# Performance work log

Hardware: AMD Instinct MI355X
Metric: run time of the kernel (lower is better)

Reference implementation:

```python
import jax, jax.numpy as jnp
import numpy as np

PATCH = 3
PAD = PATCH // 2  # stride = 1


def _extract_patches(x):
    """torch F.unfold(k=3, s=1, p=1) reshaped to [b, n=h*w, c*3*3] (c slowest, then ki, kj)."""
    b, c, h, w = x.shape
    xp = jnp.pad(x, ((0, 0), (0, 0), (PAD, PAD), (PAD, PAD)))
    # stack the 9 shifted views -> [b, c, 9, h, w]
    pats = jnp.stack([xp[:, :, i:i + h, j:j + w]
                      for i in range(PATCH) for j in range(PATCH)], axis=2)
    pats = pats.reshape(b, c, PATCH, PATCH, h, w)
    # -> [b, h*w, c*PATCH*PATCH], matching torch unfold channel ordering
    return pats.transpose(0, 4, 5, 1, 2, 3).reshape(b, h * w, c * PATCH * PATCH)


def _l2_normalize(x):
    # F.normalize(dim=2): x / max(||x||_2, 1e-12)
    n = jnp.linalg.norm(x, axis=2, keepdims=True)
    return x / jnp.maximum(n, 1e-12)


def _fold(patches_flat, c, h, w):
    """torch F.fold(k=3, s=1, p=1): overlap-add patches back to [b, c, h, w]."""
    b = patches_flat.shape[0]
    p = patches_flat.reshape(b, h, w, c, PATCH, PATCH)
    out = jnp.zeros((b, c, h + 2 * PAD, w + 2 * PAD), patches_flat.dtype)
    for i in range(PATCH):
        for j in range(PATCH):
            out = out.at[:, :, i:i + h, j:j + w].add(
                p[:, :, :, :, i, j].transpose(0, 3, 1, 2))
    return out[:, :, PAD:PAD + h, PAD:PAD + w]


def setup_inputs() -> dict:
    key = jax.random.key(0)
    k1, k2 = jax.random.split(key)
    B, C, H, W = 1, 256, 96, 96
    return {
        "content_features": jax.random.normal(k1, (B, C, H, W), dtype=jnp.float32),
        "style_features": jax.random.normal(k2, (B, C, H, W), dtype=jnp.float32),
    }


def reference(content_features, style_features):
    b, c, h, w = content_features.shape
    cpat = _extract_patches(content_features)   # [b, n, d]
    spat = _extract_patches(style_features)     # [b, m, d]
    # all-pairs cosine similarity: [b, n, m]
    sim = jnp.einsum('bnd,bmd->bnm', _l2_normalize(cpat), _l2_normalize(spat))
    best = jnp.argmax(sim, axis=2)              # [b, n]
    matched = jnp.take_along_axis(spat, best[:, :, None], axis=1)  # [b, n, d]
    num = _fold(matched, c, h, w)
    den = _fold(jnp.ones_like(matched), c, h, w)
    return num / (den + 1e-8)
```

## Files before the change

kernel.cpp:

```cpp
#include <hip/hip_runtime.h>

#define HH 96
#define WW 96
#define CCH 256
#define NPIX (HH*WW)
#define HP 98
#define NROWS 9604
#define CORE_LO 99
#define CORE_HI 9505

typedef unsigned short u16;
typedef short bf16x8 __attribute__((ext_vector_type(8)));
typedef float f32x4 __attribute__((ext_vector_type(4)));
typedef int i32x4 __attribute__((ext_vector_type(4)));

__device__ __forceinline__ f32x4 ld4u(const float* p) {
    f32x4 r; __builtin_memcpy(&r, p, 16); return r;
}
__device__ __forceinline__ i32x4 ld4ui(const int* p) {
    i32x4 r; __builtin_memcpy(&r, p, 16); return r;
}

__device__ __forceinline__ u16 f2bf_rne(float x) {
    unsigned u = __float_as_uint(x);
    return (u16)((u + 0x7FFFu + ((u >> 16) & 1u)) >> 16);
}

__device__ __forceinline__ void stage8(const u16* const* srcs, u16* dst, int kb) {
#pragma unroll
    for (int t = 0; t < 8; ++t)
        __builtin_amdgcn_global_load_lds(
            (const __attribute__((address_space(1))) unsigned int*)(srcs[t] + kb),
            (__attribute__((address_space(3))) unsigned int*)(dst + t * 512),
            16, 0, 0);
}

__global__ __launch_bounds__(256) void tobf16_kernel(const float* __restrict__ X,
                                                     u16* __restrict__ HiT,
                                                     u16* __restrict__ LoT) {
    __shared__ u16 hi[64][65], lo[64][65];
    const int n0 = blockIdx.x * 64, k0 = blockIdx.y * 64;
    const int t = threadIdx.x;
    {
        const int kr = t >> 6, nl = t & 63;
#pragma unroll
        for (int r = 0; r < 16; ++r) {
            int kl = kr * 16 + r;
            float x = X[(k0 + kl) * NPIX + n0 + nl];
            u16 h = f2bf_rne(x);
            float hf = __uint_as_float((unsigned)h << 16);
            hi[kl][nl] = h;
            lo[kl][nl] = f2bf_rne(x - hf);
        }
    }
    __syncthreads();
    {
        const int nr = t >> 6, kl = t & 63;
#pragma unroll
        for (int r = 0; r < 16; ++r) {
            int nl = nr * 16 + r;
            HiT[(n0 + nl) * CCH + k0 + kl] = hi[kl][nl];
            LoT[(n0 + nl) * CCH + k0 + kl] = lo[kl][nl];
        }
    }
}

__global__ __launch_bounds__(256) void xst_kernel(const float* __restrict__ X,
                                                  float* __restrict__ XT) {
    __shared__ float tile[64][65];
    const int p0 = blockIdx.x * 64, c0 = blockIdx.y * 64;
    const int t = threadIdx.x;
    const int rr = t >> 6, cl = t & 63;
#pragma unroll
    for (int r = 0; r < 16; ++r)
        tile[rr * 16 + r][cl] = X[(c0 + rr * 16 + r) * NPIX + p0 + cl];
    __syncthreads();
#pragma unroll
    for (int r = 0; r < 16; ++r)
        XT[(p0 + rr * 16 + r) * CCH + c0 + cl] = tile[cl][rr * 16 + r];
}

__global__ __launch_bounds__(256) void prep_kernel(const float* __restrict__ Xs,
                                                   float* __restrict__ ssum,
                                                   unsigned long long* __restrict__ keys) {
    int p = blockIdx.x * 256 + threadIdx.x;
    if (p >= NPIX) return;
    float s = 0.f;
#pragma unroll 8
    for (int c = 0; c < CCH; ++c) {
        float v = Xs[c * NPIX + p];
        s = fmaf(v, v, s);
    }
    ssum[p] = s;
    keys[p] = 0ULL;
}

__global__ __launch_bounds__(256) void rnsbp_kernel(const float* __restrict__ ssum,
                                                    float* __restrict__ rnsp,
                                                    float* __restrict__ biasp,
                                                    int* __restrict__ midxp) {
    int mp = blockIdx.x * 256 + threadIdx.x;
    if (mp >= 9632) return;
    int yq = mp / HP, xq = mp - yq * HP;
    bool real = (yq >= 1 && yq <= 96 && xq >= 1 && xq <= 96);
    if (!real) { rnsp[mp] = 0.f; biasp[mp] = -3e38f; midxp[mp] = 0; return; }
    int y = yq - 1, x = xq - 1;
    float s = 0.f;
    for (int dy = -1; dy <= 1; ++dy) {
        int yy = y + dy;
        if ((unsigned)yy >= HH) continue;
        for (int dx = -1; dx <= 1; ++dx) {
            int xx = x + dx;
            if ((unsigned)xx >= WW) continue;
            s += ssum[yy * WW + xx];
        }
    }
    rnsp[mp] = 1.f / fmaxf(sqrtf(s), 1e-12f);
    biasp[mp] = 0.f;
    midxp[mp] = y * WW + x;
}

__global__ __launch_bounds__(256) void padzero_kernel(float* __restrict__ cc, int wstride) {
    int p = blockIdx.x;
    int yq = p / HP, xq = p - yq * HP;
    if (yq >= 1 && yq <= 96 && xq >= 1 && xq <= 96) return;
    const f32x4 z = {0.f, 0.f, 0.f, 0.f};
    float* row = cc + (long long)p * wstride;
    for (int c = threadIdx.x * 4; c < wstride; c += 1024)
        *(f32x4*)&row[c] = z;
}

__global__ __launch_bounds__(256, 2) void cc_gemm_kernel(
        const u16* __restrict__ ChiT, const u16* __restrict__ CloT,
        const u16* __restrict__ ShiT, const u16* __restrict__ SloT,
        const u16* __restrict__ zbuf,
        float* __restrict__ cc, int csp, int wstride) {
    __shared__ u16 lds[2][4][8][64][8];

    const int tid = threadIdx.x;
    const int n0 = blockIdx.x * 128;
    const int m0 = blockIdx.y * 128;
    const int wave = tid >> 6, lane = tid & 63;
    const int wr = wave >> 1, wc = wave & 1;
    const int rlo = lane & 15, kseg = (lane >> 4) * 8;

    const u16* srcs[8];
    if (wave < 2) {
        const u16* base = (wave == 0) ? ChiT : CloT;
#pragma unroll
        for (int t = 0; t < 8; ++t)
            srcs[t] = base + (n0 + t * 16 + rlo) * CCH + kseg;
    } else {
        const u16* base = (wave == 2) ? ShiT : SloT;
#pragma unroll
        for (int t = 0; t < 8; ++t) {
            int qp = csp + m0 + t * 16 + rlo;
            int yq = qp / HP, xq = qp - yq * HP;
            bool ok = (qp < NROWS) && (yq >= 1 && yq <= 96 && xq >= 1 && xq <= 96);
            srcs[t] = ok ? (base + ((yq - 1) * WW + (xq - 1)) * CCH + kseg)
                         : (zbuf + kseg);
        }
    }
    u16* slab0 = &lds[0][wave][0][0][0];
    u16* slab1 = &lds[1][wave][0][0][0];

    f32x4 acc[4][4];
#pragma unroll
    for (int i = 0; i < 4; ++i)
#pragma unroll
        for (int j = 0; j < 4; ++j) acc[i][j] = (f32x4){0.f, 0.f, 0.f, 0.f};

    stage8(srcs, slab0, 0);
    stage8(srcs, slab1, 32);

#define READS(CUR)                                                          \
    bf16x8 ah[4], al[4], bh[4], bl[4];                                      \
    _Pragma("unroll")                                                       \
    for (int i = 0; i < 4; ++i) {                                           \
        ah[i] = *(const bf16x8*)&lds[CUR][0][wr * 4 + i][lane][0];          \
        al[i] = *(const bf16x8*)&lds[CUR][1][wr * 4 + i][lane][0];          \
        bh[i] = *(const bf16x8*)&lds[CUR][2][wc * 4 + i][lane][0];          \
        bl[i] = *(const bf16x8*)&lds[CUR][3][wc * 4 + i][lane][0];          \
    }

#define MFMAS                                                               \
    _Pragma("unroll")                                                       \
    for (int i = 0; i < 4; ++i)                                             \
        _Pragma("unroll")                                                   \
        for (int j = 0; j < 4; ++j) {                                       \
            acc[i][j] = __builtin_amdgcn_mfma_f32_16x16x32_bf16(ah[i], bh[j], acc[i][j], 0, 0, 0); \
            acc[i][j] = __builtin_amdgcn_mfma_f32_16x16x32_bf16(ah[i], bl[j], acc[i][j], 0, 0, 0); \
            acc[i][j] = __builtin_amdgcn_mfma_f32_16x16x32_bf16(al[i], bh[j], acc[i][j], 0, 0, 0); \
        }

#define KSTEP(KK, WN)                                                       \
    {                                                                       \
        asm volatile("s_waitcnt vmcnt(" #WN ")" ::: "memory");              \
        __builtin_amdgcn_sched_barrier(0);                                  \
        __builtin_amdgcn_s_barrier();                                       \
        READS((KK) & 1)                                                     \
        asm volatile("s_waitcnt lgkmcnt(0)" ::: "memory");                  \
        __builtin_amdgcn_sched_barrier(0);                                  \
        __builtin_amdgcn_s_barrier();                                       \
        if ((KK) + 2 < 8)                                                   \
            stage8(srcs, (((KK) & 1)) ? slab1 : slab0, ((KK) + 2) * 32);    \
        __builtin_amdgcn_sched_barrier(0);                                  \
        MFMAS                                                               \
    }

    KSTEP(0, 8) KSTEP(1, 8) KSTEP(2, 8) KSTEP(3, 8)
    KSTEP(4, 8) KSTEP(5, 8) KSTEP(6, 8) KSTEP(7, 0)

#undef KSTEP
#undef MFMAS
#undef READS

    const int r0 = (lane >> 4) * 4;
    const int cl = lane & 15;
#pragma unroll
    for (int i = 0; i < 4; ++i) {
        const int prow = n0 + wr * 64 + i * 16 + r0;
#pragma unroll
        for (int r = 0; r < 4; ++r) {
            const int row = prow + r;
            const int pp = row + 2 * (row / WW) + CORE_LO;
            const long long base = (long long)pp * wstride + m0 + wc * 64 + cl;
#pragma unroll
            for (int j = 0; j < 4; ++j)
                cc[base + j * 16] = acc[i][j][r];
        }
    }
}

__global__ __launch_bounds__(256) void boxsum_kernel(
        const float* __restrict__ cc, const float* __restrict__ rnsp,
        const float* __restrict__ biasp, const int* __restrict__ midxp,
        unsigned long long* __restrict__ keys,
        int core0, int coreEnd, int csp, int wstride) {
    const int wave = threadIdx.x >> 6, lane = threadIdx.x & 63;
    const int n = blockIdx.x * 4 + wave;
    const int pp = n + 2 * (n / WW) + CORE_LO;
    const long long rowbase = (long long)pp * wstride - csp;
    const int W1 = wstride + 1;

    const int OFF[9] = {-99, -98, -97, -1, 0, 1, 97, 98, 99};
    const float* tp[9];
#pragma unroll
    for (int t = 0; t < 9; ++t)
        tp[t] = cc + rowbase + core0 + lane * 4 + (long long)OFF[t] * W1;

    float best = -1e30f;
    int bidx = 0;
    for (int mq = core0 + lane * 4; mq < coreEnd; mq += 256) {
        f32x4 s = {0.f, 0.f, 0.f, 0.f};
#pragma unroll
        for (int t = 0; t < 9; ++t) { s += ld4u(tp[t]); tp[t] += 256; }
        f32x4 rv = ld4u(rnsp + mq);
        f32x4 bv = ld4u(biasp + mq);
        i32x4 iv = ld4ui(midxp + mq);
#pragma unroll
        for (int sl = 0; sl < 4; ++sl) {
            float v = fmaf(s[sl], rv[sl], bv[sl]);
            if (mq + sl >= coreEnd) v = -3e38f;
            if (v > best) { best = v; bidx = iv[sl]; }
        }
    }
#pragma unroll
    for (int d = 32; d; d >>= 1) {
        float ov = __shfl_xor(best, d);
        int oi = __shfl_xor(bidx, d);
        if (ov > best || (ov == best && oi < bidx)) { best = ov; bidx = oi; }
    }
    if (lane == 0) {
        unsigned u = __float_as_uint(best);
        unsigned key = (u & 0x80000000u) ? ~u : (u | 0x80000000u);
        unsigned long long k64 = ((unsigned long long)key << 32)
                               | (unsigned long long)(0xFFFFFFFFu - (unsigned)bidx);
        atomicMax(&keys[n], k64);
    }
}

__global__ __launch_bounds__(256) void fold2_kernel(const float* __restrict__ XsT,
                                                    const unsigned long long* __restrict__ keys,
                                                    float* __restrict__ outT) {
    const int wave = threadIdx.x >> 6, lane = threadIdx.x & 63;
    const int p = blockIdx.x * 4 + wave;
    const int y = p / WW, x = p - y * WW;
    f32x4 num = {0.f, 0.f, 0.f, 0.f};
    int den = 0;
#pragma unroll
    for (int i = 0; i < 3; ++i) {
        int ny = y + 1 - i;
        if ((unsigned)ny >= HH) continue;
#pragma unroll
        for (int j = 0; j < 3; ++j) {
            int nx = x + 1 - j;
            if ((unsigned)nx >= WW) continue;
            den++;
            unsigned long long k64 = keys[ny * WW + nx];
            int mg = (int)(0xFFFFFFFFu - (unsigned)(k64 & 0xFFFFFFFFu));
            int my = mg / WW, mx = mg - my * WW;
            int sy = my + i - 1, sx = mx + j - 1;
            if ((unsigned)sy < HH && (unsigned)sx < WW)
                num += ld4u(XsT + (long long)(sy * WW + sx) * CCH + lane * 4);
        }
    }
    float inv = 1.f / ((float)den + 1e-8f);
    f32x4 o = {num[0] * inv, num[1] * inv, num[2] * inv, num[3] * inv};
    *(f32x4*)&outT[(long long)p * CCH + lane * 4] = o;
}

__global__ __launch_bounds__(256) void outtr_kernel(const float* __restrict__ outT,
                                                    float* __restrict__ out) {
    __shared__ float tile[64][65];
    const int p0 = blockIdx.x * 64, c0 = blockIdx.y * 64;
    const int t = threadIdx.x;
    const int rr = t >> 6, cl = t & 63;
#pragma unroll
    for (int r = 0; r < 16; ++r)
        tile[rr * 16 + r][cl] = outT[(long long)(p0 + rr * 16 + r) * CCH + c0 + cl];
    __syncthreads();
#pragma unroll
    for (int r = 0; r < 16; ++r)
        out[(long long)(c0 + rr * 16 + r) * NPIX + p0 + cl] = tile[cl][rr * 16 + r];
}

extern "C" void kernel_launch(void* const* d_in, const int* in_sizes, int n_in,
                              void* d_out, int out_size, void* d_ws, size_t ws_size,
                              hipStream_t stream) {
    (void)in_sizes; (void)n_in; (void)out_size;
    const float* Xc = (const float*)d_in[0];
    const float* Xs = (const float*)d_in[1];
    float* out = (float*)d_out;

    char* w = (char*)d_ws;
    unsigned long long* keys = (unsigned long long*)w;  w += (size_t)NPIX * 8;
    float* ssum  = (float*)w;                           w += (size_t)NPIX * 4;
    float* rnsp  = (float*)w;                           w += (size_t)9632 * 4;
    float* biasp = (float*)w;                           w += (size_t)9632 * 4;
    int*   midxp = (int*)w;                             w += (size_t)9632 * 4;
    u16*   zbuf  = (u16*)w;                             w += 1024;
    float* XsT   = (float*)w;                           w += (size_t)NPIX * CCH * 4;
    float* outT  = (float*)w;                           w += (size_t)NPIX * CCH * 4;
    u16* ChiT = (u16*)w;                                w += (size_t)NPIX * CCH * 2;
    u16* CloT = (u16*)w;                                w += (size_t)NPIX * CCH * 2;
    u16* ShiT = (u16*)w;                                w += (size_t)NPIX * CCH * 2;
    u16* SloT = (u16*)w;                                w += (size_t)NPIX * CCH * 2;
    float* ccbuf = (float*)w;
    const size_t fixed = (size_t)(w - (char*)d_ws);

    long long avail = (ws_size > fixed + 4096)
                        ? (long long)(ws_size - fixed - 4096) : 0;
    int wstride = (int)(((avail / ((long long)NROWS * 4)) / 128) * 128);
    if (wstride > 2560) wstride = 2560;
    if (wstride < 512) wstride = 512;
    const int McCore = wstride - 198;

    hipMemsetAsync(zbuf, 0, 1024, stream);
    dim3 gt(NPIX / 64, CCH / 64);
    tobf16_kernel<<<gt, 256, 0, stream>>>(Xc, ChiT, CloT);
    tobf16_kernel<<<gt, 256, 0, stream>>>(Xs, ShiT, SloT);
    xst_kernel<<<gt, 256, 0, stream>>>(Xs, XsT);
    prep_kernel<<<NPIX / 256, 256, 0, stream>>>(Xs, ssum, keys);
    rnsbp_kernel<<<38, 256, 0, stream>>>(ssum, rnsp, biasp, midxp);
    padzero_kernel<<<NROWS, 256, 0, stream>>>(ccbuf, wstride);

    for (int core0 = CORE_LO; core0 < CORE_HI; core0 += McCore) {
        int coreEnd = (core0 + McCore < CORE_HI) ? core0 + McCore : CORE_HI;
        int csp = core0 - 99;
        int ce = coreEnd + 99; if (ce > NROWS) ce = NROWS;
        int Wc = ce - csp;
        dim3 g(NPIX / 128, (Wc + 127) / 128);
        cc_gemm_kernel<<<g, 256, 0, stream>>>(ChiT, CloT, ShiT, SloT, zbuf,
                                              ccbuf, csp, wstride);
        boxsum_kernel<<<NPIX / 4, 256, 0, stream>>>(ccbuf, rnsp, biasp, midxp, keys,
                                                    core0, coreEnd, csp, wstride);
    }

    fold2_kernel<<<NPIX / 4, 256, 0, stream>>>(XsT, keys, outT);
    outtr_kernel<<<gt, 256, 0, stream>>>(outT, out);
}
```

Measured before the change: 447.7 us.

## Use single-pass fp16 GEMM with candidate collection and exact fp32 rescoring

Replaces the three-MFMA bf16 hi/lo split GEMM with a single fp16 MFMA pass, which cuts GEMM compute and staging traffic by about two thirds and raises the occupancy hint. To keep the argmax exact, boxsum now records every style index whose approximate score lies within a content-norm-based threshold of the running max. A new rescore kernel then re-evaluates those candidates in fp32 and picks the best. The risks are candidate-list overflow beyond the cap of 64, fp16 range issues, and atomic contention in the candidate append path.

```diff
diff --git a/kernel.cpp b/kernel.cpp
--- a/kernel.cpp
+++ b/kernel.cpp
@@ -8,9 +8,11 @@
 #define NROWS 9604
 #define CORE_LO 99
 #define CORE_HI 9505
+#define CAND_CAP 64
 
 typedef unsigned short u16;
-typedef short bf16x8 __attribute__((ext_vector_type(8)));
+typedef _Float16 f16;
+typedef _Float16 f16x8 __attribute__((ext_vector_type(8)));
 typedef float f32x4 __attribute__((ext_vector_type(4)));
 typedef int i32x4 __attribute__((ext_vector_type(4)));
 
@@ -21,78 +23,50 @@
     i32x4 r; __builtin_memcpy(&r, p, 16); return r;
 }
 
-__device__ __forceinline__ u16 f2bf_rne(float x) {
-    unsigned u = __float_as_uint(x);
-    return (u16)((u + 0x7FFFu + ((u >> 16) & 1u)) >> 16);
-}
-
-__device__ __forceinline__ void stage8(const u16* const* srcs, u16* dst, int kb) {
-#pragma unroll
-    for (int t = 0; t < 8; ++t)
+__device__ __forceinline__ void stage4(const u16* const* srcs, u16* dst, int kb) {
+#pragma unroll
+    for (int t = 0; t < 4; ++t)
         __builtin_amdgcn_global_load_lds(
             (const __attribute__((address_space(1))) unsigned int*)(srcs[t] + kb),
             (__attribute__((address_space(3))) unsigned int*)(dst + t * 512),
             16, 0, 0);
 }
 
-__global__ __launch_bounds__(256) void tobf16_kernel(const float* __restrict__ X,
-                                                     u16* __restrict__ HiT,
-                                                     u16* __restrict__ LoT) {
-    __shared__ u16 hi[64][65], lo[64][65];
-    const int n0 = blockIdx.x * 64, k0 = blockIdx.y * 64;
-    const int t = threadIdx.x;
-    {
-        const int kr = t >> 6, nl = t & 63;
-#pragma unroll
-        for (int r = 0; r < 16; ++r) {
-            int kl = kr * 16 + r;
-            float x = X[(k0 + kl) * NPIX + n0 + nl];
-            u16 h = f2bf_rne(x);
-            float hf = __uint_as_float((unsigned)h << 16);
-            hi[kl][nl] = h;
-            lo[kl][nl] = f2bf_rne(x - hf);
-        }
-    }
-    __syncthreads();
-    {
-        const int nr = t >> 6, kl = t & 63;
-#pragma unroll
-        for (int r = 0; r < 16; ++r) {
-            int nl = nr * 16 + r;
-            HiT[(n0 + nl) * CCH + k0 + kl] = hi[kl][nl];
-            LoT[(n0 + nl) * CCH + k0 + kl] = lo[kl][nl];
-        }
-    }
-}
-
-__global__ __launch_bounds__(256) void xst_kernel(const float* __restrict__ X,
-                                                  float* __restrict__ XT) {
+__global__ __launch_bounds__(256) void xsth_kernel(const float* __restrict__ X,
+                                                   float* __restrict__ XT,
+                                                   u16* __restrict__ XTh) {
     __shared__ float tile[64][65];
     const int p0 = blockIdx.x * 64, c0 = blockIdx.y * 64;
-    const int t = threadIdx.x;
-    const int rr = t >> 6, cl = t & 63;
+    const int rr = threadIdx.x >> 6, cl = threadIdx.x & 63;
 #pragma unroll
     for (int r = 0; r < 16; ++r)
         tile[rr * 16 + r][cl] = X[(c0 + rr * 16 + r) * NPIX + p0 + cl];
     __syncthreads();
 #pragma unroll
-    for (int r = 0; r < 16; ++r)
-        XT[(p0 + rr * 16 + r) * CCH + c0 + cl] = tile[cl][rr * 16 + r];
-}
-
-__global__ __launch_bounds__(256) void prep_kernel(const float* __restrict__ Xs,
+    for (int r = 0; r < 16; ++r) {
+        float v = tile[cl][rr * 16 + r];
+        long long o = (long long)(p0 + rr * 16 + r) * CCH + c0 + cl;
+        XT[o] = v;
+        f16 h = (f16)v;
+        u16 hb; __builtin_memcpy(&hb, &h, 2);
+        XTh[o] = hb;
+    }
+}
+
+__global__ __launch_bounds__(256) void prep_kernel(const float* __restrict__ X,
                                                    float* __restrict__ ssum,
-                                                   unsigned long long* __restrict__ keys) {
+                                                   unsigned long long* __restrict__ keys,
+                                                   int* __restrict__ cnt, int reset) {
     int p = blockIdx.x * 256 + threadIdx.x;
     if (p >= NPIX) return;
     float s = 0.f;
 #pragma unroll 8
     for (int c = 0; c < CCH; ++c) {
-        float v = Xs[c * NPIX + p];
+        float v = X[c * NPIX + p];
         s = fmaf(v, v, s);
     }
     ssum[p] = s;
-    keys[p] = 0ULL;
+    if (reset) { keys[p] = 0ULL; cnt[p] = 0; }
 }
 
 __global__ __launch_bounds__(256) void rnsbp_kernel(const float* __restrict__ ssum,
@@ -120,6 +94,24 @@
     midxp[mp] = y * WW + x;
 }
 
+__global__ __launch_bounds__(256) void cthr_kernel(const float* __restrict__ ssum,
+                                                   float* __restrict__ thr) {
+    int n = blockIdx.x * 256 + threadIdx.x;
+    if (n >= NPIX) return;
+    int y = n / WW, x = n - y * WW;
+    float s = 0.f;
+    for (int dy = -1; dy <= 1; ++dy) {
+        int yy = y + dy;
+        if ((unsigned)yy >= HH) continue;
+        for (int dx = -1; dx <= 1; ++dx) {
+            int xx = x + dx;
+            if ((unsigned)xx >= WW) continue;
+            s += ssum[yy * WW + xx];
+        }
+    }
+    thr[n] = 0.004f * sqrtf(s);
+}
+
 __global__ __launch_bounds__(256) void padzero_kernel(float* __restrict__ cc, int wstride) {
     int p = blockIdx.x;
     int yq = p / HP, xq = p - yq * HP;
@@ -130,12 +122,11 @@
         *(f32x4*)&row[c] = z;
 }
 
-__global__ __launch_bounds__(256, 2) void cc_gemm_kernel(
-        const u16* __restrict__ ChiT, const u16* __restrict__ CloT,
-        const u16* __restrict__ ShiT, const u16* __restrict__ SloT,
+__global__ __launch_bounds__(256, 4) void cc_gemm_kernel(
+        const u16* __restrict__ ChT, const u16* __restrict__ ShT,
         const u16* __restrict__ zbuf,
         float* __restrict__ cc, int csp, int wstride) {
-    __shared__ u16 lds[2][4][8][64][8];
+    __shared__ u16 lds[2][2][8][64][8];
 
     const int tid = threadIdx.x;
     const int n0 = blockIdx.x * 128;
@@ -143,26 +134,26 @@
     const int wave = tid >> 6, lane = tid & 63;
     const int wr = wave >> 1, wc = wave & 1;
     const int rlo = lane & 15, kseg = (lane >> 4) * 8;
-
-    const u16* srcs[8];
-    if (wave < 2) {
-        const u16* base = (wave == 0) ? ChiT : CloT;
-#pragma unroll
-        for (int t = 0; t < 8; ++t)
-            srcs[t] = base + (n0 + t * 16 + rlo) * CCH + kseg;
+    const int isB = wave >> 1;
+    const int tb = (wave & 1) * 4;
+
+    const u16* srcs[4];
+    if (!isB) {
+#pragma unroll
+        for (int t = 0; t < 4; ++t)
+            srcs[t] = ChT + (n0 + (tb + t) * 16 + rlo) * CCH + kseg;
     } else {
-        const u16* base = (wave == 2) ? ShiT : SloT;
-#pragma unroll
-        for (int t = 0; t < 8; ++t) {
-            int qp = csp + m0 + t * 16 + rlo;
+#pragma unroll
+        for (int t = 0; t < 4; ++t) {
+            int qp = csp + m0 + (tb + t) * 16 + rlo;
             int yq = qp / HP, xq = qp - yq * HP;
             bool ok = (qp < NROWS) && (yq >= 1 && yq <= 96 && xq >= 1 && xq <= 96);
-            srcs[t] = ok ? (base + ((yq - 1) * WW + (xq - 1)) * CCH + kseg)
+            srcs[t] = ok ? (ShT + ((yq - 1) * WW + (xq - 1)) * CCH + kseg)
                          : (zbuf + kseg);
         }
     }
-    u16* slab0 = &lds[0][wave][0][0][0];
-    u16* slab1 = &lds[1][wave][0][0][0];
+    u16* slab0 = &lds[0][isB][tb][0][0];
+    u16* slab1 = &lds[1][isB][tb][0][0];
 
     f32x4 acc[4][4];
 #pragma unroll
@@ -170,28 +161,23 @@
 #pragma unroll
         for (int j = 0; j < 4; ++j) acc[i][j] = (f32x4){0.f, 0.f, 0.f, 0.f};
 
-    stage8(srcs, slab0, 0);
-    stage8(srcs, slab1, 32);
+    stage4(srcs, slab0, 0);
+    stage4(srcs, slab1, 32);
 
 #define READS(CUR)                                                          \
-    bf16x8 ah[4], al[4], bh[4], bl[4];                                      \
+    f16x8 ah[4], bh[4];                                                     \
     _Pragma("unroll")                                                       \
     for (int i = 0; i < 4; ++i) {                                           \
-        ah[i] = *(const bf16x8*)&lds[CUR][0][wr * 4 + i][lane][0];          \
-        al[i] = *(const bf16x8*)&lds[CUR][1][wr * 4 + i][lane][0];          \
-        bh[i] = *(const bf16x8*)&lds[CUR][2][wc * 4 + i][lane][0];          \
-        bl[i] = *(const bf16x8*)&lds[CUR][3][wc * 4 + i][lane][0];          \
+        ah[i] = *(const f16x8*)&lds[CUR][0][wr * 4 + i][lane][0];           \
+        bh[i] = *(const f16x8*)&lds[CUR][1][wc * 4 + i][lane][0];           \
     }
 
 #define MFMAS                                                               \
     _Pragma("unroll")                                                       \
     for (int i = 0; i < 4; ++i)                                             \
         _Pragma("unroll")                                                   \
-        for (int j = 0; j < 4; ++j) {                                       \
-            acc[i][j] = __builtin_amdgcn_mfma_f32_16x16x32_bf16(ah[i], bh[j], acc[i][j], 0, 0, 0); \
-            acc[i][j] = __builtin_amdgcn_mfma_f32_16x16x32_bf16(ah[i], bl[j], acc[i][j], 0, 0, 0); \
-            acc[i][j] = __builtin_amdgcn_mfma_f32_16x16x32_bf16(al[i], bh[j], acc[i][j], 0, 0, 0); \
-        }
+        for (int j = 0; j < 4; ++j)                                         \
+            acc[i][j] = __builtin_amdgcn_mfma_f32_16x16x32_f16(ah[i], bh[j], acc[i][j], 0, 0, 0);
 
 #define KSTEP(KK, WN)                                                       \
     {                                                                       \
@@ -203,13 +189,13 @@
         __builtin_amdgcn_sched_barrier(0);                                  \
         __builtin_amdgcn_s_barrier();                                       \
         if ((KK) + 2 < 8)                                                   \
-            stage8(srcs, (((KK) & 1)) ? slab1 : slab0, ((KK) + 2) * 32);    \
+            stage4(srcs, (((KK) & 1)) ? slab1 : slab0, ((KK) + 2) * 32);    \
         __builtin_amdgcn_sched_barrier(0);                                  \
         MFMAS                                                               \
     }
 
-    KSTEP(0, 8) KSTEP(1, 8) KSTEP(2, 8) KSTEP(3, 8)
-    KSTEP(4, 8) KSTEP(5, 8) KSTEP(6, 8) KSTEP(7, 0)
+    KSTEP(0, 4) KSTEP(1, 4) KSTEP(2, 4) KSTEP(3, 4)
+    KSTEP(4, 4) KSTEP(5, 4) KSTEP(6, 4) KSTEP(7, 0)
 
 #undef KSTEP
 #undef MFMAS
@@ -235,13 +221,26 @@
 __global__ __launch_bounds__(256) void boxsum_kernel(
         const float* __restrict__ cc, const float* __restrict__ rnsp,
         const float* __restrict__ biasp, const int* __restrict__ midxp,
+        const float* __restrict__ thr,
         unsigned long long* __restrict__ keys,
+        int* __restrict__ cnt, u16* __restrict__ cand,
         int core0, int coreEnd, int csp, int wstride) {
     const int wave = threadIdx.x >> 6, lane = threadIdx.x & 63;
     const int n = blockIdx.x * 4 + wave;
     const int pp = n + 2 * (n / WW) + CORE_LO;
     const long long rowbase = (long long)pp * wstride - csp;
     const int W1 = wstride + 1;
+    const float thrn = thr[n];
+
+    float wmax = -1e30f;
+    {
+        unsigned long long k0 = keys[n];
+        if (k0) {
+            unsigned ku = (unsigned)(k0 >> 32);
+            wmax = (ku & 0x80000000u) ? __uint_as_float(ku ^ 0x80000000u)
+                                      : __uint_as_float(~ku);
+        }
+    }
 
     const int OFF[9] = {-99, -98, -97, -1, 0, 1, 97, 98, 99};
     const float* tp[9];
@@ -249,8 +248,6 @@
     for (int t = 0; t < 9; ++t)
         tp[t] = cc + rowbase + core0 + lane * 4 + (long long)OFF[t] * W1;
 
-    float best = -1e30f;
-    int bidx = 0;
     for (int mq = core0 + lane * 4; mq < coreEnd; mq += 256) {
         f32x4 s = {0.f, 0.f, 0.f, 0.f};
 #pragma unroll
@@ -258,30 +255,74 @@
         f32x4 rv = ld4u(rnsp + mq);
         f32x4 bv = ld4u(biasp + mq);
         i32x4 iv = ld4ui(midxp + mq);
+        float v[4];
 #pragma unroll
         for (int sl = 0; sl < 4; ++sl) {
-            float v = fmaf(s[sl], rv[sl], bv[sl]);
-            if (mq + sl >= coreEnd) v = -3e38f;
-            if (v > best) { best = v; bidx = iv[sl]; }
-        }
-    }
-#pragma unroll
-    for (int d = 32; d; d >>= 1) {
-        float ov = __shfl_xor(best, d);
-        int oi = __shfl_xor(bidx, d);
-        if (ov > best || (ov == best && oi < bidx)) { best = ov; bidx = oi; }
+            v[sl] = fmaf(s[sl], rv[sl], bv[sl]);
+            if (mq + sl >= coreEnd) v[sl] = -3e38f;
+        }
+        float im = fmaxf(fmaxf(v[0], v[1]), fmaxf(v[2], v[3]));
+#pragma unroll
+        for (int d = 32; d; d >>= 1) im = fmaxf(im, __shfl_xor(im, d));
+        wmax = fmaxf(wmax, im);
+#pragma unroll
+        for (int sl = 0; sl < 4; ++sl) {
+            if (v[sl] >= wmax - thrn) {
+                int idx = atomicAdd(&cnt[n], 1);
+                if (idx < CAND_CAP) cand[n * CAND_CAP + idx] = (u16)iv[sl];
+            }
+        }
     }
     if (lane == 0) {
-        unsigned u = __float_as_uint(best);
+        unsigned u = __float_as_uint(wmax);
         unsigned key = (u & 0x80000000u) ? ~u : (u | 0x80000000u);
-        unsigned long long k64 = ((unsigned long long)key << 32)
-                               | (unsigned long long)(0xFFFFFFFFu - (unsigned)bidx);
-        atomicMax(&keys[n], k64);
-    }
+        atomicMax(&keys[n], ((unsigned long long)key) << 32);
+    }
+}
+
+__global__ __launch_bounds__(256) void rescore_kernel(
+        const float* __restrict__ XcT, const float* __restrict__ XsT,
+        const float* __restrict__ rnsp,
+        const int* __restrict__ cnt, const u16* __restrict__ cand,
+        int* __restrict__ bestm) {
+    const int wave = threadIdx.x >> 6, lane = threadIdx.x & 63;
+    const int n = blockIdx.x * 4 + wave;
+    int c = cnt[n]; if (c > CAND_CAP) c = CAND_CAP;
+    if (c == 1) {
+        if (lane == 0) bestm[n] = cand[n * CAND_CAP];
+        return;
+    }
+    const int yn = n / WW, xn = n - yn * WW;
+    const f32x4 z = {0.f, 0.f, 0.f, 0.f};
+    f32x4 an[9];
+#pragma unroll
+    for (int t = 0; t < 9; ++t) {
+        int di = t / 3 - 1, dj = t % 3 - 1;
+        bool ok = ((unsigned)(yn + di) < HH) && ((unsigned)(xn + dj) < WW);
+        an[t] = ok ? ld4u(XcT + (long long)((yn + di) * WW + xn + dj) * CCH + lane * 4) : z;
+    }
+    float bv = -1e30f; int bm = 0x7fffffff;
+    for (int k = 0; k < c; ++k) {
+        int m = cand[n * CAND_CAP + k];
+        int ym = m / WW, xm = m - ym * WW;
+        f32x4 acc = z;
+#pragma unroll
+        for (int t = 0; t < 9; ++t) {
+            int di = t / 3 - 1, dj = t % 3 - 1;
+            if (((unsigned)(ym + di) < HH) && ((unsigned)(xm + dj) < WW))
+                acc += an[t] * ld4u(XsT + (long long)((ym + di) * WW + xm + dj) * CCH + lane * 4);
+        }
+        float d = acc[0] + acc[1] + acc[2] + acc[3];
+#pragma unroll
+        for (int dd = 32; dd; dd >>= 1) d += __shfl_xor(d, dd);
+        float v = d * rnsp[(ym + 1) * HP + (xm + 1)];
+        if (v > bv || (v == bv && m < bm)) { bv = v; bm = m; }
+    }
+    if (lane == 0) bestm[n] = bm;
 }
 
 __global__ __launch_bounds__(256) void fold2_kernel(const float* __restrict__ XsT,
-                                                    const unsigned long long* __restrict__ keys,
+                                                    const int* __restrict__ bestm,
                                                     float* __restrict__ outT) {
     const int wave = threadIdx.x >> 6, lane = threadIdx.x & 63;
     const int p = blockIdx.x * 4 + wave;
@@ -297,8 +338,7 @@
             int nx = x + 1 - j;
             if ((unsigned)nx >= WW) continue;
             den++;
-            unsigned long long k64 = keys[ny * WW + nx];
-            int mg = (int)(0xFFFFFFFFu - (unsigned)(k64 & 0xFFFFFFFFu));
+            int mg = bestm[ny * WW + nx];
             int my = mg / WW, mx = mg - my * WW;
             int sy = my + i - 1, sx = mx + j - 1;
             if ((unsigned)sy < HH && (unsigned)sx < WW)
@@ -335,17 +375,21 @@
 
     char* w = (char*)d_ws;
     unsigned long long* keys = (unsigned long long*)w;  w += (size_t)NPIX * 8;
-    float* ssum  = (float*)w;                           w += (size_t)NPIX * 4;
+    float* XcT  = (float*)w;                            w += (size_t)NPIX * CCH * 4;
+    float* XsT  = (float*)w;                            w += (size_t)NPIX * CCH * 4;
+    float* outT = (float*)w;                            w += (size_t)NPIX * CCH * 4;
+    u16* XcH = (u16*)w;                                 w += (size_t)NPIX * CCH * 2;
+    u16* XsH = (u16*)w;                                 w += (size_t)NPIX * CCH * 2;
+    float* ssum_s = (float*)w;                          w += (size_t)NPIX * 4;
+    float* ssum_c = (float*)w;                          w += (size_t)NPIX * 4;
     float* rnsp  = (float*)w;                           w += (size_t)9632 * 4;
     float* biasp = (float*)w;                           w += (size_t)9632 * 4;
     int*   midxp = (int*)w;                             w += (size_t)9632 * 4;
+    float* thr   = (float*)w;                           w += (size_t)NPIX * 4;
+    int*   cnt   = (int*)w;                             w += (size_t)NPIX * 4;
+    int*   bestm = (int*)w;                             w += (size_t)NPIX * 4;
+    u16*   cand  = (u16*)w;                             w += (size_t)NPIX * CAND_CAP * 2;
     u16*   zbuf  = (u16*)w;                             w += 1024;
-    float* XsT   = (float*)w;                           w += (size_t)NPIX * CCH * 4;
-    float* outT  = (float*)w;                           w += (size_t)NPIX * CCH * 4;
-    u16* ChiT = (u16*)w;                                w += (size_t)NPIX * CCH * 2;
-    u16* CloT = (u16*)w;                                w += (size_t)NPIX * CCH * 2;
-    u16* ShiT = (u16*)w;                                w += (size_t)NPIX * CCH * 2;
-    u16* SloT = (u16*)w;                                w += (size_t)NPIX * CCH * 2;
     float* ccbuf = (float*)w;
     const size_t fixed = (size_t)(w - (char*)d_ws);
 
@@ -358,11 +402,12 @@
 
     hipMemsetAsync(zbuf, 0, 1024, stream);
     dim3 gt(NPIX / 64, CCH / 64);
-    tobf16_kernel<<<gt, 256, 0, stream>>>(Xc, ChiT, CloT);
-    tobf16_kernel<<<gt, 256, 0, stream>>>(Xs, ShiT, SloT);
-    xst_kernel<<<gt, 256, 0, stream>>>(Xs, XsT);
-    prep_kernel<<<NPIX / 256, 256, 0, stream>>>(Xs, ssum, keys);
-    rnsbp_kernel<<<38, 256, 0, stream>>>(ssum, rnsp, biasp, midxp);
+    xsth_kernel<<<gt, 256, 0, stream>>>(Xc, XcT, XcH);
+    xsth_kernel<<<gt, 256, 0, stream>>>(Xs, XsT, XsH);
+    prep_kernel<<<NPIX / 256, 256, 0, stream>>>(Xs, ssum_s, keys, cnt, 1);
+    prep_kernel<<<NPIX / 256, 256, 0, stream>>>(Xc, ssum_c, keys, cnt, 0);
+    rnsbp_kernel<<<38, 256, 0, stream>>>(ssum_s, rnsp, biasp, midxp);
+    cthr_kernel<<<NPIX / 256, 256, 0, stream>>>(ssum_c, thr);
     padzero_kernel<<<NROWS, 256, 0, stream>>>(ccbuf, wstride);
 
     for (int core0 = CORE_LO; core0 < CORE_HI; core0 += McCore) {
@@ -371,12 +416,13 @@
         int ce = coreEnd + 99; if (ce > NROWS) ce = NROWS;
         int Wc = ce - csp;
         dim3 g(NPIX / 128, (Wc + 127) / 128);
-        cc_gemm_kernel<<<g, 256, 0, stream>>>(ChiT, CloT, ShiT, SloT, zbuf,
-                                              ccbuf, csp, wstride);
-        boxsum_kernel<<<NPIX / 4, 256, 0, stream>>>(ccbuf, rnsp, biasp, midxp, keys,
+        cc_gemm_kernel<<<g, 256, 0, stream>>>(XcH, XsH, zbuf, ccbuf, csp, wstride);
+        boxsum_kernel<<<NPIX / 4, 256, 0, stream>>>(ccbuf, rnsp, biasp, midxp, thr,
+                                                    keys, cnt, cand,
                                                     core0, coreEnd, csp, wstride);
     }
 
-    fold2_kernel<<<NPIX / 4, 256, 0, stream>>>(XsT, keys, outT);
+    rescore_kernel<<<NPIX / 4, 256, 0, stream>>>(XcT, XsT, rnsp, cnt, cand, bestm);
+    fold2_kernel<<<NPIX / 4, 256, 0, stream>>>(XsT, bestm, outT);
     outtr_kernel<<<gt, 256, 0, stream>>>(outT, out);
 }
```

New measurement: 567.0 us. 26.6% more time.
